# Optimization experiments

Measured on AMD Instinct MI355X. Metric: run time of the kernel, lower is better.

## Reference

```python
import jax, jax.numpy as jnp
import numpy as np

N_NODES = 100000
N_EDGES = 3200000
IN_DIM, HID_DIM, N_CLASSES = 128, 64, 8


def setup_inputs() -> dict:
    key = jax.random.key(0)
    k1, k2, k3, k4, k5 = jax.random.split(key, 5)
    x = jax.random.normal(k1, (N_NODES, IN_DIM), dtype=jnp.float32)
    src = jax.random.randint(k2, (N_EDGES,), 0, N_NODES, dtype=jnp.int32)
    dst = jax.random.randint(k3, (N_EDGES,), 0, N_NODES, dtype=jnp.int32)
    W1 = jax.random.normal(k4, (IN_DIM, HID_DIM), dtype=jnp.float32) / np.sqrt(IN_DIM)
    b1 = jnp.zeros((HID_DIM,), dtype=jnp.float32)
    W2 = jax.random.normal(k5, (HID_DIM, N_CLASSES), dtype=jnp.float32) / np.sqrt(HID_DIM)
    b2 = jnp.zeros((N_CLASSES,), dtype=jnp.float32)
    return {"x": x, "src": src, "dst": dst, "W1": W1, "b1": b1, "W2": W2, "b2": b2}


def _graph_conv(x, src, dst, W, b, out_norm, in_norm, n_nodes):
    # DGL GraphConv norm='both': h = D_in^{-1/2} A (D_out^{-1/2} x) W + b
    h = x * out_norm[:, None]
    h = h @ W  # project first (smaller message width when out < in)
    msgs = h[src]  # gather along edges: [E, out_dim]
    agg = jax.ops.segment_sum(msgs, dst, num_segments=n_nodes)
    return agg * in_norm[:, None] + b


def reference(x, src, dst, W1, b1, W2, b2):
    n = x.shape[0]
    ones_e = jnp.ones(src.shape[0], dtype=x.dtype)
    out_deg = jnp.clip(jax.ops.segment_sum(ones_e, src, num_segments=n), 1.0)
    in_deg = jnp.clip(jax.ops.segment_sum(ones_e, dst, num_segments=n), 1.0)
    out_norm = jax.lax.rsqrt(out_deg)
    in_norm = jax.lax.rsqrt(in_deg)
    h = _graph_conv(x, src, dst, W1, b1, out_norm, in_norm, n)
    h = jax.nn.relu(h)
    h = _graph_conv(h, src, dst, W2, b2, out_norm, in_norm, n)
    return jax.nn.softmax(h, axis=1)
```

## Files before the change

### kernel.cpp

```cpp
#include <hip/hip_runtime.h>
#include <hip/hip_bf16.h>


#define IN_DIM 128
#define HID 64
#define NC 8
#define BH 128
#define TPB 1024
#define BINS 33792
#define XS_LD 132

__global__ __launch_bounds__(TPB) void histcnt_k(const int* __restrict__ keys,
                                                 int* __restrict__ cnt, int e, int n) {
    __shared__ int bins[BINS];
    int b = blockIdx.x;
    int chunk = (e + gridDim.x - 1) / gridDim.x;
    int beg = b * chunk, end = min(e, beg + chunk);
    for (int rb = 0; rb < n; rb += BINS) {
        int hi = min(n - rb, BINS);
        for (int i = threadIdx.x; i < hi; i += TPB) bins[i] = 0;
        __syncthreads();
        for (int i = beg + threadIdx.x; i < end; i += TPB) {
            int k = keys[i] - rb;
            if ((unsigned)k < (unsigned)hi) atomicAdd(&bins[k], 1);
        }
        __syncthreads();
        for (int i = threadIdx.x; i < hi; i += TPB)
            cnt[(size_t)b * n + rb + i] = bins[i];
        __syncthreads();
    }
}

__global__ void redout_k(const int* __restrict__ cnt, float* __restrict__ out_norm, int n) {
    int v = blockIdx.x * blockDim.x + threadIdx.x;
    if (v >= n) return;
    int s = 0;
    for (int b = 0; b < BH; ++b) s += cnt[(size_t)b * n + v];
    out_norm[v] = rsqrtf(fmaxf((float)s, 1.0f));
}

__global__ void redin_k(int* __restrict__ cnt, float* __restrict__ in_norm,
                        int* __restrict__ indeg, int n) {
    int v = blockIdx.x * blockDim.x + threadIdx.x;
    if (v >= n) return;
    int run = 0;
    for (int b = 0; b < BH; ++b) {
        size_t idx = (size_t)b * n + v;
        int c = cnt[idx];
        cnt[idx] = run;
        run += c;
    }
    indeg[v] = run;
    in_norm[v] = rsqrtf(fmaxf((float)run, 1.0f));
}

__global__ void scanA(const int* __restrict__ indeg, int* __restrict__ bsum, int n) {
    int t = threadIdx.x;
    int i = blockIdx.x * 256 + t;
    int v = (i < n) ? indeg[i] : 0;
#pragma unroll
    for (int d = 1; d < 64; d <<= 1) v += __shfl_xor(v, d, 64);
    __shared__ int w4[4];
    if ((t & 63) == 0) w4[t >> 6] = v;
    __syncthreads();
    if (t == 0) bsum[blockIdx.x] = w4[0] + w4[1] + w4[2] + w4[3];
}

__global__ void scanB(int* __restrict__ bsum, int nb, int* __restrict__ rowptr, int n) {
    __shared__ int s[512];
    int t = threadIdx.x;
    s[t] = (t < nb) ? bsum[t] : 0;
    __syncthreads();
    for (int d = 1; d < 512; d <<= 1) {
        int v = (t >= d) ? s[t - d] : 0;
        __syncthreads();
        s[t] += v;
        __syncthreads();
    }
    if (t < nb) bsum[t] = t ? s[t - 1] : 0;
    if (t == 0) rowptr[n] = s[nb - 1];
}

__global__ void scanC(const int* __restrict__ indeg, const int* __restrict__ bsum,
                      int* __restrict__ rowptr, int n) {
    __shared__ int s[256];
    int t = threadIdx.x;
    int i = blockIdx.x * 256 + t;
    int v = (i < n) ? indeg[i] : 0;
    s[t] = v;
    __syncthreads();
    for (int d = 1; d < 256; d <<= 1) {
        int u = (t >= d) ? s[t - d] : 0;
        __syncthreads();
        s[t] += u;
        __syncthreads();
    }
    if (i < n) rowptr[i] = bsum[blockIdx.x] + s[t] - v;
}

__global__ __launch_bounds__(TPB) void fill2_k(const int* __restrict__ src, const int* __restrict__ dst,
                        const int* __restrict__ rowptr, const int* __restrict__ base,
                        int* __restrict__ csr, int e, int n) {
    __shared__ int cur[BINS];
    int b = blockIdx.x;
    int chunk = (e + gridDim.x - 1) / gridDim.x;
    int beg = b * chunk, end = min(e, beg + chunk);
    for (int rb = 0; rb < n; rb += BINS) {
        int hi = min(n - rb, BINS);
        for (int i = threadIdx.x; i < hi; i += TPB) cur[i] = 0;
        __syncthreads();
        for (int i = beg + threadIdx.x; i < end; i += TPB) {
            int d = dst[i];
            int dl = d - rb;
            if ((unsigned)dl < (unsigned)hi) {
                int slot = rowptr[d] + base[(size_t)b * n + d] + atomicAdd(&cur[dl], 1);
                csr[slot] = src[i];
            }
        }
        __syncthreads();
    }
}

__global__ __launch_bounds__(256) void gemm1_k(const float* __restrict__ x, const float* __restrict__ W1,
                        const float* __restrict__ out_norm, float* __restrict__ h0, int n) {
    __shared__ float xs[64 * XS_LD];
    __shared__ float Ws[IN_DIM * HID];
    int t = threadIdx.x;
    int row0 = blockIdx.x * 64;
#pragma unroll
    for (int j = 0; j < 8; ++j) {
        int f4 = t + j * 256;
        *(float4*)&Ws[f4 * 4] = ((const float4*)W1)[f4];
    }
#pragma unroll
    for (int j = 0; j < 8; ++j) {
        int f4 = t + j * 256;
        int r = f4 >> 5;
        int k = (f4 & 31) * 4;
        float4 v = (row0 + r < n) ? ((const float4*)x)[(size_t)(row0 + r) * 32 + (f4 & 31)]
                                  : make_float4(0.f, 0.f, 0.f, 0.f);
        *(float4*)&xs[r * XS_LD + k] = v;
    }
    __syncthreads();
    int rq = (t >> 4) * 4;
    int cq = (t & 15) * 4;
    float acc[4][4] = {};
    for (int k = 0; k < IN_DIM; k += 4) {
        float4 xr[4], wc[4];
#pragma unroll
        for (int i = 0; i < 4; ++i) xr[i] = *(const float4*)&xs[(rq + i) * XS_LD + k];
#pragma unroll
        for (int kk = 0; kk < 4; ++kk) wc[kk] = *(const float4*)&Ws[(k + kk) * HID + cq];
#pragma unroll
        for (int i = 0; i < 4; ++i) {
            float xv0 = xr[i].x, xv1 = xr[i].y, xv2 = xr[i].z, xv3 = xr[i].w;
            acc[i][0] += xv0 * wc[0].x + xv1 * wc[1].x + xv2 * wc[2].x + xv3 * wc[3].x;
            acc[i][1] += xv0 * wc[0].y + xv1 * wc[1].y + xv2 * wc[2].y + xv3 * wc[3].y;
            acc[i][2] += xv0 * wc[0].z + xv1 * wc[1].z + xv2 * wc[2].z + xv3 * wc[3].z;
            acc[i][3] += xv0 * wc[0].w + xv1 * wc[1].w + xv2 * wc[2].w + xv3 * wc[3].w;
        }
    }
#pragma unroll
    for (int i = 0; i < 4; ++i) {
        int row = row0 + rq + i;
        if (row < n) {
            float onn = out_norm[row];
            float4 o = make_float4(acc[i][0] * onn, acc[i][1] * onn, acc[i][2] * onn, acc[i][3] * onn);
            *(float4*)&h0[(size_t)row * HID + cq] = o;
        }
    }
}

__global__ void agg1proj_k(const int* __restrict__ rowptr, const int* __restrict__ csr,
                           const float* __restrict__ h0, const float* __restrict__ in_norm,
                           const float* __restrict__ out_norm, const float* __restrict__ b1,
                           const float* __restrict__ W2, float* __restrict__ h2p, int n) {
    int wid = (blockIdx.x * blockDim.x + threadIdx.x) >> 6;
    int lane = threadIdx.x & 63;
    if (wid >= n) return;
    int beg = rowptr[wid], end = rowptr[wid + 1];
    float acc0 = 0.f, acc1 = 0.f, acc2 = 0.f, acc3 = 0.f;
    int j = beg;
    for (; j + 8 <= end; j += 8) {
        int s0 = csr[j],     s1 = csr[j + 1], s2 = csr[j + 2], s3 = csr[j + 3];
        int s4 = csr[j + 4], s5 = csr[j + 5], s6 = csr[j + 6], s7 = csr[j + 7];
        float a0 = h0[(size_t)s0 * HID + lane];
        float a1 = h0[(size_t)s1 * HID + lane];
        float a2 = h0[(size_t)s2 * HID + lane];
        float a3 = h0[(size_t)s3 * HID + lane];
        float a4 = h0[(size_t)s4 * HID + lane];
        float a5 = h0[(size_t)s5 * HID + lane];
        float a6 = h0[(size_t)s6 * HID + lane];
        float a7 = h0[(size_t)s7 * HID + lane];
        acc0 += a0; acc1 += a1; acc2 += a2; acc3 += a3;
        acc0 += a4; acc1 += a5; acc2 += a6; acc3 += a7;
    }
    if (j + 4 <= end) {
        int s0 = csr[j], s1 = csr[j + 1], s2 = csr[j + 2], s3 = csr[j + 3];
        acc0 += h0[(size_t)s0 * HID + lane];
        acc1 += h0[(size_t)s1 * HID + lane];
        acc2 += h0[(size_t)s2 * HID + lane];
        acc3 += h0[(size_t)s3 * HID + lane];
        j += 4;
    }
    for (; j < end; ++j) acc0 += h0[(size_t)csr[j] * HID + lane];
    float acc = (acc0 + acc1) + (acc2 + acc3);
    float v = fmaxf(acc * in_norm[wid] + b1[lane], 0.f);
    float onn = out_norm[wid];
    float res = 0.f;
#pragma unroll
    for (int c = 0; c < NC; ++c) {
        float p = v * W2[lane * NC + c];
        p += __shfl_xor(p, 1, 64);
        p += __shfl_xor(p, 2, 64);
        p += __shfl_xor(p, 4, 64);
        p += __shfl_xor(p, 8, 64);
        p += __shfl_xor(p, 16, 64);
        p += __shfl_xor(p, 32, 64);
        if (lane == c) res = p;
    }
    if (lane < NC) h2p[(size_t)wid * NC + lane] = onn * res;
}

__global__ void agg2smax_k(const int* __restrict__ rowptr, const int* __restrict__ csr,
                           const float* __restrict__ h2p, const float* __restrict__ in_norm,
                           const float* __restrict__ b2, float* __restrict__ out, int n) {
    int wid = (blockIdx.x * blockDim.x + threadIdx.x) >> 6;
    int lane = threadIdx.x & 63;
    if (wid >= n) return;
    int beg = rowptr[wid], end = rowptr[wid + 1];
    int c = lane & 7, e8 = lane >> 3;
    float acc0 = 0.f, acc1 = 0.f;
    int j = beg + e8;
    for (; j + 8 < end; j += 16) {
        int s0 = csr[j];
        int s1 = csr[j + 8];
        acc0 += h2p[(size_t)s0 * NC + c];
        acc1 += h2p[(size_t)s1 * NC + c];
    }
    for (; j < end; j += 8) acc0 += h2p[(size_t)csr[j] * NC + c];
    float acc = acc0 + acc1;
    acc += __shfl_xor(acc, 8, 64);
    acc += __shfl_xor(acc, 16, 64);
    acc += __shfl_xor(acc, 32, 64);
    float v = acc * in_norm[wid] + b2[c];
    float m = v;
    m = fmaxf(m, __shfl_xor(m, 1, 64));
    m = fmaxf(m, __shfl_xor(m, 2, 64));
    m = fmaxf(m, __shfl_xor(m, 4, 64));
    float ev = __expf(v - m);
    float s8 = ev;
    s8 += __shfl_xor(s8, 1, 64);
    s8 += __shfl_xor(s8, 2, 64);
    s8 += __shfl_xor(s8, 4, 64);
    if (e8 == 0) out[(size_t)wid * NC + c] = ev / s8;
}

extern "C" void kernel_launch(void* const* d_in, const int* in_sizes, int n_in,
                              void* d_out, int out_size, void* d_ws, size_t ws_size,
                              hipStream_t stream) {
    const float* x   = (const float*)d_in[0];
    const int*   src = (const int*)d_in[1];
    const int*   dst = (const int*)d_in[2];
    const float* W1  = (const float*)d_in[3];
    const float* b1  = (const float*)d_in[4];
    const float* W2  = (const float*)d_in[5];
    const float* b2  = (const float*)d_in[6];
    float* out = (float*)d_out;

    const int N = in_sizes[0] / IN_DIM;
    const int E = in_sizes[1];
    const int NB = (N + 255) / 256;

    float* ws = (float*)d_ws;
    float* out_norm = ws;
    float* in_norm  = ws + (size_t)N;
    int*   indeg    = (int*)(ws + (size_t)2 * N);
    int*   rowptr   = indeg + N;
    int*   bsum     = rowptr + (N + 1);
    int*   csr      = bsum + 512;
    int*   cnt      = csr + E;
    float* h0       = (float*)cnt;
    float* h2p      = (float*)cnt + (size_t)64 * N;

    histcnt_k<<<BH, TPB, 0, stream>>>(src, cnt, E, N);
    redout_k<<<(N + 255) / 256, 256, 0, stream>>>(cnt, out_norm, N);
    histcnt_k<<<BH, TPB, 0, stream>>>(dst, cnt, E, N);
    redin_k<<<(N + 255) / 256, 256, 0, stream>>>(cnt, in_norm, indeg, N);
    scanA<<<NB, 256, 0, stream>>>(indeg, bsum, N);
    scanB<<<1, 512, 0, stream>>>(bsum, NB, rowptr, N);
    scanC<<<NB, 256, 0, stream>>>(indeg, bsum, rowptr, N);
    fill2_k<<<BH, TPB, 0, stream>>>(src, dst, rowptr, cnt, csr, E, N);
    gemm1_k<<<(N + 63) / 64, 256, 0, stream>>>(x, W1, out_norm, h0, N);
    agg1proj_k<<<(N + 3) / 4, 256, 0, stream>>>(rowptr, csr, h0, in_norm, out_norm, b1, W2, h2p, N);
    agg2smax_k<<<(N + 3) / 4, 256, 0, stream>>>(rowptr, csr, h2p, in_norm, b2, out, N);
}
```

Measured before the change: 547.4 us.

## Store projected layer-1 features as bf16 and preload per-block fill offsets

The projected hidden features h0 are now written in bf16 instead of fp32. This halves the bytes gathered per edge in the layer-1 aggregation, which is the dominant random-gather cost. Separately, fill2_k seeds its shared counters from the per-block base offsets, removing one global load per edge. The bf16 rounding of messages may loosen accuracy against the fp32 reference, and per-lane 2-byte loads give only 128-byte rows per gather.

```diff
diff --git a/kernel.cpp b/kernel.cpp
--- a/kernel.cpp
+++ b/kernel.cpp
@@ -9,6 +9,15 @@
 #define TPB 1024
 #define BINS 33792
 #define XS_LD 132
+
+__device__ __forceinline__ unsigned short f2bf(float f) {
+    unsigned int x = __float_as_uint(f);
+    x += 0x7fffu + ((x >> 16) & 1u);
+    return (unsigned short)(x >> 16);
+}
+__device__ __forceinline__ float bf2f(unsigned short u) {
+    return __uint_as_float(((unsigned int)u) << 16);
+}
 
 __global__ __launch_bounds__(TPB) void histcnt_k(const int* __restrict__ keys,
                                                  int* __restrict__ cnt, int e, int n) {
@@ -107,13 +116,14 @@
     int beg = b * chunk, end = min(e, beg + chunk);
     for (int rb = 0; rb < n; rb += BINS) {
         int hi = min(n - rb, BINS);
-        for (int i = threadIdx.x; i < hi; i += TPB) cur[i] = 0;
+        for (int i = threadIdx.x; i < hi; i += TPB)
+            cur[i] = base[(size_t)b * n + rb + i];
         __syncthreads();
         for (int i = beg + threadIdx.x; i < end; i += TPB) {
             int d = dst[i];
             int dl = d - rb;
             if ((unsigned)dl < (unsigned)hi) {
-                int slot = rowptr[d] + base[(size_t)b * n + d] + atomicAdd(&cur[dl], 1);
+                int slot = rowptr[d] + atomicAdd(&cur[dl], 1);
                 csr[slot] = src[i];
             }
         }
@@ -122,7 +132,7 @@
 }
 
 __global__ __launch_bounds__(256) void gemm1_k(const float* __restrict__ x, const float* __restrict__ W1,
-                        const float* __restrict__ out_norm, float* __restrict__ h0, int n) {
+                        const float* __restrict__ out_norm, unsigned short* __restrict__ h0, int n) {
     __shared__ float xs[64 * XS_LD];
     __shared__ float Ws[IN_DIM * HID];
     int t = threadIdx.x;
@@ -165,14 +175,18 @@
         int row = row0 + rq + i;
         if (row < n) {
             float onn = out_norm[row];
-            float4 o = make_float4(acc[i][0] * onn, acc[i][1] * onn, acc[i][2] * onn, acc[i][3] * onn);
-            *(float4*)&h0[(size_t)row * HID + cq] = o;
+            ushort4 o;
+            o.x = f2bf(acc[i][0] * onn);
+            o.y = f2bf(acc[i][1] * onn);
+            o.z = f2bf(acc[i][2] * onn);
+            o.w = f2bf(acc[i][3] * onn);
+            *(ushort4*)&h0[(size_t)row * HID + cq] = o;
         }
     }
 }
 
 __global__ void agg1proj_k(const int* __restrict__ rowptr, const int* __restrict__ csr,
-                           const float* __restrict__ h0, const float* __restrict__ in_norm,
+                           const unsigned short* __restrict__ h0, const float* __restrict__ in_norm,
                            const float* __restrict__ out_norm, const float* __restrict__ b1,
                            const float* __restrict__ W2, float* __restrict__ h2p, int n) {
     int wid = (blockIdx.x * blockDim.x + threadIdx.x) >> 6;
@@ -184,26 +198,26 @@
     for (; j + 8 <= end; j += 8) {
         int s0 = csr[j],     s1 = csr[j + 1], s2 = csr[j + 2], s3 = csr[j + 3];
         int s4 = csr[j + 4], s5 = csr[j + 5], s6 = csr[j + 6], s7 = csr[j + 7];
-        float a0 = h0[(size_t)s0 * HID + lane];
-        float a1 = h0[(size_t)s1 * HID + lane];
-        float a2 = h0[(size_t)s2 * HID + lane];
-        float a3 = h0[(size_t)s3 * HID + lane];
-        float a4 = h0[(size_t)s4 * HID + lane];
-        float a5 = h0[(size_t)s5 * HID + lane];
-        float a6 = h0[(size_t)s6 * HID + lane];
-        float a7 = h0[(size_t)s7 * HID + lane];
-        acc0 += a0; acc1 += a1; acc2 += a2; acc3 += a3;
-        acc0 += a4; acc1 += a5; acc2 += a6; acc3 += a7;
+        unsigned short a0 = h0[(size_t)s0 * HID + lane];
+        unsigned short a1 = h0[(size_t)s1 * HID + lane];
+        unsigned short a2 = h0[(size_t)s2 * HID + lane];
+        unsigned short a3 = h0[(size_t)s3 * HID + lane];
+        unsigned short a4 = h0[(size_t)s4 * HID + lane];
+        unsigned short a5 = h0[(size_t)s5 * HID + lane];
+        unsigned short a6 = h0[(size_t)s6 * HID + lane];
+        unsigned short a7 = h0[(size_t)s7 * HID + lane];
+        acc0 += bf2f(a0); acc1 += bf2f(a1); acc2 += bf2f(a2); acc3 += bf2f(a3);
+        acc0 += bf2f(a4); acc1 += bf2f(a5); acc2 += bf2f(a6); acc3 += bf2f(a7);
     }
     if (j + 4 <= end) {
         int s0 = csr[j], s1 = csr[j + 1], s2 = csr[j + 2], s3 = csr[j + 3];
-        acc0 += h0[(size_t)s0 * HID + lane];
-        acc1 += h0[(size_t)s1 * HID + lane];
-        acc2 += h0[(size_t)s2 * HID + lane];
-        acc3 += h0[(size_t)s3 * HID + lane];
+        acc0 += bf2f(h0[(size_t)s0 * HID + lane]);
+        acc1 += bf2f(h0[(size_t)s1 * HID + lane]);
+        acc2 += bf2f(h0[(size_t)s2 * HID + lane]);
+        acc3 += bf2f(h0[(size_t)s3 * HID + lane]);
         j += 4;
     }
-    for (; j < end; ++j) acc0 += h0[(size_t)csr[j] * HID + lane];
+    for (; j < end; ++j) acc0 += bf2f(h0[(size_t)csr[j] * HID + lane]);
     float acc = (acc0 + acc1) + (acc2 + acc3);
     float v = fmaxf(acc * in_norm[wid] + b1[lane], 0.f);
     float onn = out_norm[wid];
@@ -280,8 +294,8 @@
     int*   bsum     = rowptr + (N + 1);
     int*   csr      = bsum + 512;
     int*   cnt      = csr + E;
-    float* h0       = (float*)cnt;
-    float* h2p      = (float*)cnt + (size_t)64 * N;
+    unsigned short* h0b = (unsigned short*)cnt;
+    float* h2p      = (float*)(cnt + (size_t)32 * N);
 
     histcnt_k<<<BH, TPB, 0, stream>>>(src, cnt, E, N);
     redout_k<<<(N + 255) / 256, 256, 0, stream>>>(cnt, out_norm, N);
@@ -291,7 +305,7 @@
     scanB<<<1, 512, 0, stream>>>(bsum, NB, rowptr, N);
     scanC<<<NB, 256, 0, stream>>>(indeg, bsum, rowptr, N);
     fill2_k<<<BH, TPB, 0, stream>>>(src, dst, rowptr, cnt, csr, E, N);
-    gemm1_k<<<(N + 63) / 64, 256, 0, stream>>>(x, W1, out_norm, h0, N);
-    agg1proj_k<<<(N + 3) / 4, 256, 0, stream>>>(rowptr, csr, h0, in_norm, out_norm, b1, W2, h2p, N);
+    gemm1_k<<<(N + 63) / 64, 256, 0, stream>>>(x, W1, out_norm, h0b, N);
+    agg1proj_k<<<(N + 3) / 4, 256, 0, stream>>>(rowptr, csr, h0b, in_norm, out_norm, b1, W2, h2p, N);
     agg2smax_k<<<(N + 3) / 4, 256, 0, stream>>>(rowptr, csr, h2p, in_norm, b2, out, N);
 }
```

New measurement: 472.6 us. -13.7%, faster.
